# Kernel tuning notes

Measured on AMD Instinct MI355X. Metric: run time of the kernel, lower is better.

## Reference

```python
import jax, jax.numpy as jnp
import numpy as np

FP16_MIN = -65504.0
FP16_MAX = 65504.0

B, S, D, H = 2, 2048, 1024, 16
HD = D // H


def setup_inputs() -> dict:
    key = jax.random.key(0)
    ks = jax.random.split(key, 12)
    s = 0.02
    inp = {
        "x_q": jax.random.normal(ks[0], (B, S, D), jnp.float32),
        "x_k": jax.random.normal(ks[1], (B, S, D), jnp.float32),
        "x_v": jax.random.normal(ks[2], (B, S, D), jnp.float32),
        # causal mask [B, 1, S, S]; 0 entries are masked out
        "mask": jnp.broadcast_to(jnp.tril(jnp.ones((S, S), jnp.int32)), (B, 1, S, S)),
        "Wq": jax.random.normal(ks[3], (D, D), jnp.float32) * s,
        "bq": jnp.zeros((D,), jnp.float32),
        "Wk": jax.random.normal(ks[4], (D, D), jnp.float32) * s,
        "bk": jnp.zeros((D,), jnp.float32),
        "Wv": jax.random.normal(ks[5], (D, D), jnp.float32) * s,
        "bv": jnp.zeros((D,), jnp.float32),
        "Wo": jax.random.normal(ks[6], (D, D), jnp.float32) * s,
        "bo": jnp.zeros((D,), jnp.float32),
    }
    return inp


def _split_heads(x):
    # [B, S, D] -> [B, H, S, HD]
    b, s, _ = x.shape
    return x.reshape(b, s, H, HD).transpose(0, 2, 1, 3)


def reference(x_q, x_k, x_v, mask, Wq, bq, Wk, bk, Wv, bv, Wo, bo):
    scale = jnp.sqrt(jnp.float32(HD))
    q = _split_heads(x_q @ Wq + bq)  # [B,H,S,HD]
    k = _split_heads(x_k @ Wk + bk)
    v = _split_heads(x_v @ Wv + bv)

    scores = jnp.einsum("bhqd,bhkd->bhqk", q, k) / scale  # [B,H,S,S]
    scores = jnp.where(mask == 0, FP16_MIN, scores)
    scores = jnp.where(jnp.isneginf(scores), FP16_MIN, scores)
    scores = jnp.where(jnp.isposinf(scores), FP16_MAX, scores)

    probs = jax.nn.softmax(scores, axis=-1)  # dropout p=0.0 -> identity
    ctx = jnp.einsum("bhqk,bhkd->bhqd", probs, v)  # [B,H,S,HD]
    ctx = ctx.transpose(0, 2, 1, 3).reshape(x_q.shape[0], x_q.shape[1], D)
    out = ctx @ Wo + bo
    return out, probs
```

## Files before the change

kernel.cpp:

```cpp
#include <hip/hip_runtime.h>


typedef __bf16 bf16x8 __attribute__((ext_vector_type(8)));
typedef float f32x4 __attribute__((ext_vector_type(4)));

__device__ __forceinline__ unsigned short f2bf(float f) {
  unsigned int u = __builtin_bit_cast(unsigned int, f);
  u += 0x7fffu + ((u >> 16) & 1u);
  return (unsigned short)(u >> 16);
}
__device__ __forceinline__ unsigned short f2bf_hw(float f) {
  return __builtin_bit_cast(unsigned short, (__bf16)f);
}
__device__ __forceinline__ float bf2f_lo(unsigned int u) {
  return __builtin_bit_cast(float, u << 16);
}
__device__ __forceinline__ float bf2f_hi(unsigned int u) {
  return __builtin_bit_cast(float, u & 0xffff0000u);
}

__global__ void transpose_w(const float* __restrict__ W0, const float* __restrict__ W1,
                            const float* __restrict__ W2, const float* __restrict__ W3,
                            unsigned short* __restrict__ Wt) {
  __shared__ float t[32][33];
  const int z = blockIdx.z;
  const float* W = (z == 0) ? W0 : (z == 1) ? W1 : (z == 2) ? W2 : W3;
  unsigned short* o = Wt + (size_t)z * 1048576u;
  const int n0 = blockIdx.x * 32, k0 = blockIdx.y * 32;
  const int tx = threadIdx.x, ty = threadIdx.y;
#pragma unroll
  for (int i = 0; i < 4; i++)
    t[ty + 8 * i][tx] = W[(size_t)(k0 + ty + 8 * i) * 1024 + n0 + tx];
  __syncthreads();
#pragma unroll
  for (int i = 0; i < 4; i++)
    o[(size_t)(n0 + ty + 8 * i) * 1024 + k0 + tx] = f2bf(t[tx][ty + 8 * i]);
}

__global__ __launch_bounds__(256) void gemm_kernel(
    const void* __restrict__ A0, const void* __restrict__ A1, const void* __restrict__ A2,
    const unsigned short* __restrict__ Wtb,
    const float* __restrict__ b0, const float* __restrict__ b1, const float* __restrict__ b2,
    void* __restrict__ O0, void* __restrict__ O1, void* __restrict__ O2,
    const int mode0) {
  __shared__ unsigned short Alds[64 * 72];
  const int z = blockIdx.z;
  const int mode = mode0 + z;
  const void* Av = (z == 0) ? A0 : (z == 1) ? A1 : A2;
  const float* bias = (z == 0) ? b0 : (z == 1) ? b1 : b2;
  void* outv = (z == 0) ? O0 : (z == 1) ? O1 : O2;
  const unsigned short* Wt = Wtb + (size_t)z * 1048576u;

  const int tid = threadIdx.x;
  const int lane = tid & 63;
  const int wave = tid >> 6;
  const int wm = wave >> 1, wn = wave & 1;
  const int m0 = blockIdx.y * 64, n0 = blockIdx.x * 128;
  const int g = lane >> 4, c = lane & 15;

  f32x4 acc[2][4];
#pragma unroll
  for (int i = 0; i < 2; i++)
#pragma unroll
    for (int j = 0; j < 4; j++) acc[i][j] = (f32x4){0.f, 0.f, 0.f, 0.f};

  const int srow = tid >> 2;
  const int sch = (tid & 3) * 16;

  uint4 pk0, pk1;
#define LOAD_PACK(KB)                                                             \
  if (mode < 3) {                                                                 \
    const float* A = (const float*)Av;                                            \
    const float4* src = (const float4*)(A + (size_t)(m0 + srow) * 1024 + (KB) + sch); \
    const float4 v0 = src[0], v1 = src[1], v2 = src[2], v3 = src[3];              \
    pk0.x = (unsigned int)f2bf(v0.x) | ((unsigned int)f2bf(v0.y) << 16);          \
    pk0.y = (unsigned int)f2bf(v0.z) | ((unsigned int)f2bf(v0.w) << 16);          \
    pk0.z = (unsigned int)f2bf(v1.x) | ((unsigned int)f2bf(v1.y) << 16);          \
    pk0.w = (unsigned int)f2bf(v1.z) | ((unsigned int)f2bf(v1.w) << 16);          \
    pk1.x = (unsigned int)f2bf(v2.x) | ((unsigned int)f2bf(v2.y) << 16);          \
    pk1.y = (unsigned int)f2bf(v2.z) | ((unsigned int)f2bf(v2.w) << 16);          \
    pk1.z = (unsigned int)f2bf(v3.x) | ((unsigned int)f2bf(v3.y) << 16);          \
    pk1.w = (unsigned int)f2bf(v3.z) | ((unsigned int)f2bf(v3.w) << 16);          \
  } else {                                                                        \
    const unsigned short* A = (const unsigned short*)Av;                          \
    const uint4* src = (const uint4*)(A + (size_t)(m0 + srow) * 1024 + (KB) + sch); \
    pk0 = src[0];                                                                 \
    pk1 = src[1];                                                                 \
  }

  LOAD_PACK(0);
  for (int kb = 0; kb < 1024; kb += 64) {
    *(uint4*)&Alds[srow * 72 + sch] = pk0;
    *(uint4*)&Alds[srow * 72 + sch + 8] = pk1;
    if (kb + 64 < 1024) { LOAD_PACK(kb + 64); }
    __syncthreads();

    bf16x8 af[2][2], bfr[4][2];
#pragma unroll
    for (int mi = 0; mi < 2; mi++)
#pragma unroll
      for (int kk = 0; kk < 2; kk++)
        af[mi][kk] = *(const bf16x8*)&Alds[(wm * 32 + mi * 16 + c) * 72 + kk * 32 + g * 8];
#pragma unroll
    for (int nf = 0; nf < 4; nf++)
#pragma unroll
      for (int kk = 0; kk < 2; kk++)
        bfr[nf][kk] = *(const bf16x8*)(Wt + (size_t)(n0 + wn * 64 + nf * 16 + c) * 1024 + kb + kk * 32 + g * 8);
#pragma unroll
    for (int kk = 0; kk < 2; kk++)
#pragma unroll
      for (int mi = 0; mi < 2; mi++)
#pragma unroll
        for (int nf = 0; nf < 4; nf++)
          acc[mi][nf] = __builtin_amdgcn_mfma_f32_16x16x32_bf16(af[mi][kk], bfr[nf][kk], acc[mi][nf], 0, 0, 0);
    __syncthreads();
  }
#undef LOAD_PACK

#pragma unroll
  for (int nf = 0; nf < 4; nf++) {
    const int col = n0 + wn * 64 + nf * 16 + c;
    const float bc = bias[col];
#pragma unroll
    for (int mi = 0; mi < 2; mi++) {
#pragma unroll
      for (int r = 0; r < 4; r++) {
        const int row = m0 + wm * 32 + mi * 16 + g * 4 + r;
        const float v = acc[mi][nf][r] + bc;
        if (mode == 0) {
          ((unsigned short*)outv)[(size_t)row * 1024 + col] = f2bf(v * 0.1803368801111244f);
        } else if (mode == 1) {
          ((unsigned short*)outv)[(size_t)row * 1024 + col] = f2bf(v);
        } else if (mode == 2) {
          const int bb = row >> 11, s = row & 2047;
          ((unsigned short*)outv)[((size_t)(bb * 1024 + col)) * 2048 + s] = f2bf(v);
        } else {
          ((float*)outv)[(size_t)row * 1024 + col] = v;
        }
      }
    }
  }
}

__global__ __launch_bounds__(512, 4) void attn_kernel(
    const unsigned short* __restrict__ Q, const unsigned short* __restrict__ K,
    const unsigned short* __restrict__ Vt, float* __restrict__ probs,
    unsigned short* __restrict__ ctx) {
  __shared__ unsigned short Klds[2][64 * 72];
  __shared__ unsigned short Vlds[2][64 * 72];
  __shared__ unsigned short Plds[128 * 72];

  const int tid = threadIdx.x;
  const int lane = tid & 63, wave = tid >> 6;
  const int g = lane >> 4, c = lane & 15;
  const int bh = blockIdx.x;
  const int b = bh >> 4, h = bh & 15;
  const int q0 = (int)(gridDim.y - 1 - blockIdx.y) * 128;
  const int qrow0 = q0 + wave * 16;
  const int wave_kend = qrow0 + 16;

  const unsigned short* Qh = Q + ((size_t)(b * 2048 + qrow0)) * 1024 + h * 64;
  const unsigned short* Kh = K + ((size_t)b * 2048) * 1024 + h * 64;
  const unsigned short* Vh = Vt + ((size_t)bh) * 64 * 2048;
  float* Ph = probs + ((size_t)(bh * 2048 + q0)) * 2048;

  const bf16x8 qa0 = *(const bf16x8*)&Qh[(size_t)c * 1024 + g * 8];
  const bf16x8 qa1 = *(const bf16x8*)&Qh[(size_t)c * 1024 + 32 + g * 8];

  const int srow = tid >> 3;
  const int scol = (tid & 7) * 8;
  const int kb_end = q0 + 128;

  float lp[4] = {0.f, 0.f, 0.f, 0.f};
  f32x4 cacc[4];
#pragma unroll
  for (int nf = 0; nf < 4; nf++) cacc[nf] = (f32x4){0.f, 0.f, 0.f, 0.f};

  const int prow = lane >> 2;
  const int pcb = (lane & 3) * 16;
  unsigned short* PwOut = (unsigned short*)Ph + (size_t)(wave * 16 + prow) * 4096 + pcb;
  const unsigned short* PwLds = &Plds[(wave * 16 + prow) * 72 + pcb];

  {
    *(uint4*)&Klds[0][srow * 72 + scol] = *(const uint4*)(Kh + (size_t)srow * 1024 + scol);
    *(uint4*)&Vlds[0][srow * 72 + scol] = *(const uint4*)(Vh + (size_t)srow * 2048 + scol);
  }

  int cur = 0;
  for (int kb = 0; kb < kb_end; kb += 64, cur ^= 1) {
    uint4 kn, vn;
    const bool more = (kb + 64) < kb_end;
    if (more) {
      kn = *(const uint4*)(Kh + (size_t)(kb + 64 + srow) * 1024 + scol);
      vn = *(const uint4*)(Vh + (size_t)srow * 2048 + kb + 64 + scol);
    }
    __syncthreads();
    if (more) {
      *(uint4*)&Klds[cur ^ 1][srow * 72 + scol] = kn;
      *(uint4*)&Vlds[cur ^ 1][srow * 72 + scol] = vn;
    }

    if (kb < wave_kend) {
      f32x4 sv[4];
#pragma unroll
      for (int sub = 0; sub < 4; sub++) {
        sv[sub] = (f32x4){0.f, 0.f, 0.f, 0.f};
        const unsigned short* Kr = &Klds[cur][(sub * 16 + c) * 72];
        sv[sub] = __builtin_amdgcn_mfma_f32_16x16x32_bf16(qa0, *(const bf16x8*)&Kr[g * 8], sv[sub], 0, 0, 0);
        sv[sub] = __builtin_amdgcn_mfma_f32_16x16x32_bf16(qa1, *(const bf16x8*)&Kr[32 + g * 8], sv[sub], 0, 0, 0);
      }
      if (kb + 63 > qrow0) {
#pragma unroll
        for (int sub = 0; sub < 4; sub++)
#pragma unroll
          for (int r = 0; r < 4; r++)
            if (kb + sub * 16 + c > qrow0 + g * 4 + r) sv[sub][r] = -1e30f;
      }
#pragma unroll
      for (int sub = 0; sub < 4; sub++)
#pragma unroll
        for (int r = 0; r < 4; r++) {
          const float pu = __builtin_amdgcn_exp2f(sv[sub][r]);
          lp[r] += pu;
          Plds[(wave * 16 + g * 4 + r) * 72 + sub * 16 + c] = f2bf_hw(pu);
        }
      const bf16x8 pa0 = *(const bf16x8*)&Plds[(wave * 16 + c) * 72 + g * 8];
      const bf16x8 pa1 = *(const bf16x8*)&Plds[(wave * 16 + c) * 72 + 32 + g * 8];
#pragma unroll
      for (int nf = 0; nf < 4; nf++) {
        const bf16x8 vf0 = *(const bf16x8*)&Vlds[cur][(nf * 16 + c) * 72 + g * 8];
        const bf16x8 vf1 = *(const bf16x8*)&Vlds[cur][(nf * 16 + c) * 72 + 32 + g * 8];
        cacc[nf] = __builtin_amdgcn_mfma_f32_16x16x32_bf16(pa0, vf0, cacc[nf], 0, 0, 0);
        cacc[nf] = __builtin_amdgcn_mfma_f32_16x16x32_bf16(pa1, vf1, cacc[nf], 0, 0, 0);
      }
      unsigned short* dst = PwOut + kb;
      *(uint4*)dst = *(const uint4*)PwLds;
      *(uint4*)(dst + 8) = *(const uint4*)(PwLds + 8);
    } else {
      unsigned short* dst = PwOut + kb;
      *(uint4*)dst = make_uint4(0u, 0u, 0u, 0u);
      *(uint4*)(dst + 8) = make_uint4(0u, 0u, 0u, 0u);
    }
  }

#pragma unroll
  for (int off = 1; off < 16; off <<= 1)
#pragma unroll
    for (int r = 0; r < 4; r++) lp[r] += __shfl_xor(lp[r], off);
  float invl[4];
#pragma unroll
  for (int r = 0; r < 4; r++) invl[r] = 1.0f / lp[r];

#pragma unroll
  for (int nf = 0; nf < 4; nf++)
#pragma unroll
    for (int r = 0; r < 4; r++)
      ctx[((size_t)(b * 2048 + qrow0 + g * 4 + r)) * 1024 + h * 64 + nf * 16 + c] =
          f2bf_hw(cacc[nf][r] * invl[r]);
}

__global__ __launch_bounds__(256) void norm_probs(float* __restrict__ probs) {
  __shared__ float wsum[4];
  const int rowIdx = blockIdx.x;
  const int q = rowIdx & 2047;
  const int kbe = ((q >> 7) + 1) << 7;
  float* base = probs + (size_t)rowIdx * 2048;
  const int t = threadIdx.x;
  const int c0 = t * 8;

  uint4 raw = make_uint4(0u, 0u, 0u, 0u);
  if (c0 < kbe) raw = *(const uint4*)((const unsigned short*)base + c0);
  float f0 = bf2f_lo(raw.x), f1 = bf2f_hi(raw.x), f2 = bf2f_lo(raw.y), f3 = bf2f_hi(raw.y);
  float f4 = bf2f_lo(raw.z), f5 = bf2f_hi(raw.z), f6 = bf2f_lo(raw.w), f7 = bf2f_hi(raw.w);

  float s = ((f0 + f1) + (f2 + f3)) + ((f4 + f5) + (f6 + f7));
#pragma unroll
  for (int off = 1; off < 64; off <<= 1) s += __shfl_xor(s, off);
  if ((t & 63) == 0) wsum[t >> 6] = s;
  __syncthreads();
  const float il = 1.0f / (wsum[0] + wsum[1] + wsum[2] + wsum[3]);

  float4* dst = (float4*)(base + c0);
  dst[0] = make_float4(f0 * il, f1 * il, f2 * il, f3 * il);
  dst[1] = make_float4(f4 * il, f5 * il, f6 * il, f7 * il);
}

extern "C" void kernel_launch(void* const* d_in, const int* in_sizes, int n_in,
                              void* d_out, int out_size, void* d_ws, size_t ws_size,
                              hipStream_t stream) {
  if (ws_size < (size_t)40 * 1024 * 1024) return;

  const float* xq = (const float*)d_in[0];
  const float* xk = (const float*)d_in[1];
  const float* xv = (const float*)d_in[2];
  const float* Wq = (const float*)d_in[4];
  const float* bq = (const float*)d_in[5];
  const float* Wk = (const float*)d_in[6];
  const float* bk = (const float*)d_in[7];
  const float* Wv = (const float*)d_in[8];
  const float* bv = (const float*)d_in[9];
  const float* Wo = (const float*)d_in[10];
  const float* bo = (const float*)d_in[11];

  unsigned short* ws = (unsigned short*)d_ws;
  unsigned short* Wt = ws;
  unsigned short* Qw = ws + (size_t)4 * 1048576u;
  unsigned short* Kw = Qw + 4194304u;
  unsigned short* Vtw = Kw + 4194304u;
  unsigned short* Cw = Vtw + 4194304u;

  float* out = (float*)d_out;
  float* probs = out + 4194304u;

  transpose_w<<<dim3(32, 32, 4), dim3(32, 8), 0, stream>>>(Wq, Wk, Wv, Wo, Wt);
  gemm_kernel<<<dim3(8, 64, 3), 256, 0, stream>>>(xq, xk, xv, Wt, bq, bk, bv,
                                                  Qw, Kw, Vtw, 0);
  attn_kernel<<<dim3(32, 16, 1), 512, 0, stream>>>(Qw, Kw, Vtw, probs, Cw);
  norm_probs<<<dim3(65536), 256, 0, stream>>>(probs);
  gemm_kernel<<<dim3(8, 64, 1), 256, 0, stream>>>(Cw, Cw, Cw, Wt + 3u * 1048576u,
                                                  bo, bo, bo, out, out, out, 3);
}
```

Baseline: 353.6 us.

## Merge output projection GEMM with probs normalization into one launch

New measurement: 381.3 us. 7.8% more time.

```diff
diff --git a/kernel.cpp b/kernel.cpp
--- a/kernel.cpp
+++ b/kernel.cpp
@@ -37,18 +37,17 @@
     o[(size_t)(n0 + ty + 8 * i) * 1024 + k0 + tx] = f2bf(t[tx][ty + 8 * i]);
 }
 
-__global__ __launch_bounds__(256) void gemm_kernel(
-    const void* __restrict__ A0, const void* __restrict__ A1, const void* __restrict__ A2,
+__global__ __launch_bounds__(256) void gemm_qkv(
+    const float* __restrict__ A0, const float* __restrict__ A1, const float* __restrict__ A2,
     const unsigned short* __restrict__ Wtb,
     const float* __restrict__ b0, const float* __restrict__ b1, const float* __restrict__ b2,
-    void* __restrict__ O0, void* __restrict__ O1, void* __restrict__ O2,
-    const int mode0) {
+    unsigned short* __restrict__ O0, unsigned short* __restrict__ O1,
+    unsigned short* __restrict__ O2) {
   __shared__ unsigned short Alds[64 * 72];
   const int z = blockIdx.z;
-  const int mode = mode0 + z;
-  const void* Av = (z == 0) ? A0 : (z == 1) ? A1 : A2;
+  const float* A = (z == 0) ? A0 : (z == 1) ? A1 : A2;
   const float* bias = (z == 0) ? b0 : (z == 1) ? b1 : b2;
-  void* outv = (z == 0) ? O0 : (z == 1) ? O1 : O2;
+  unsigned short* outv = (z == 0) ? O0 : (z == 1) ? O1 : O2;
   const unsigned short* Wt = Wtb + (size_t)z * 1048576u;
 
   const int tid = threadIdx.x;
@@ -69,8 +68,7 @@
 
   uint4 pk0, pk1;
 #define LOAD_PACK(KB)                                                             \
-  if (mode < 3) {                                                                 \
-    const float* A = (const float*)Av;                                            \
+  {                                                                               \
     const float4* src = (const float4*)(A + (size_t)(m0 + srow) * 1024 + (KB) + sch); \
     const float4 v0 = src[0], v1 = src[1], v2 = src[2], v3 = src[3];              \
     pk0.x = (unsigned int)f2bf(v0.x) | ((unsigned int)f2bf(v0.y) << 16);          \
@@ -81,11 +79,6 @@
     pk1.y = (unsigned int)f2bf(v2.z) | ((unsigned int)f2bf(v2.w) << 16);          \
     pk1.z = (unsigned int)f2bf(v3.x) | ((unsigned int)f2bf(v3.y) << 16);          \
     pk1.w = (unsigned int)f2bf(v3.z) | ((unsigned int)f2bf(v3.w) << 16);          \
-  } else {                                                                        \
-    const unsigned short* A = (const unsigned short*)Av;                          \
-    const uint4* src = (const uint4*)(A + (size_t)(m0 + srow) * 1024 + (KB) + sch); \
-    pk0 = src[0];                                                                 \
-    pk1 = src[1];                                                                 \
   }
 
   LOAD_PACK(0);
@@ -127,15 +120,13 @@
       for (int r = 0; r < 4; r++) {
         const int row = m0 + wm * 32 + mi * 16 + g * 4 + r;
         const float v = acc[mi][nf][r] + bc;
-        if (mode == 0) {
-          ((unsigned short*)outv)[(size_t)row * 1024 + col] = f2bf(v * 0.1803368801111244f);
-        } else if (mode == 1) {
-          ((unsigned short*)outv)[(size_t)row * 1024 + col] = f2bf(v);
-        } else if (mode == 2) {
+        if (z == 0) {
+          outv[(size_t)row * 1024 + col] = f2bf(v * 0.1803368801111244f);
+        } else if (z == 1) {
+          outv[(size_t)row * 1024 + col] = f2bf(v);
+        } else {
           const int bb = row >> 11, s = row & 2047;
-          ((unsigned short*)outv)[((size_t)(bb * 1024 + col)) * 2048 + s] = f2bf(v);
-        } else {
-          ((float*)outv)[(size_t)row * 1024 + col] = v;
+          outv[((size_t)(bb * 1024 + col)) * 2048 + s] = f2bf(v);
         }
       }
     }
@@ -259,30 +250,97 @@
           f2bf_hw(cacc[nf][r] * invl[r]);
 }
 
-__global__ __launch_bounds__(256) void norm_probs(float* __restrict__ probs) {
-  __shared__ float wsum[4];
-  const int rowIdx = blockIdx.x;
-  const int q = rowIdx & 2047;
-  const int kbe = ((q >> 7) + 1) << 7;
-  float* base = probs + (size_t)rowIdx * 2048;
-  const int t = threadIdx.x;
-  const int c0 = t * 8;
-
-  uint4 raw = make_uint4(0u, 0u, 0u, 0u);
-  if (c0 < kbe) raw = *(const uint4*)((const unsigned short*)base + c0);
-  float f0 = bf2f_lo(raw.x), f1 = bf2f_hi(raw.x), f2 = bf2f_lo(raw.y), f3 = bf2f_hi(raw.y);
-  float f4 = bf2f_lo(raw.z), f5 = bf2f_hi(raw.z), f6 = bf2f_lo(raw.w), f7 = bf2f_hi(raw.w);
-
-  float s = ((f0 + f1) + (f2 + f3)) + ((f4 + f5) + (f6 + f7));
-#pragma unroll
-  for (int off = 1; off < 64; off <<= 1) s += __shfl_xor(s, off);
-  if ((t & 63) == 0) wsum[t >> 6] = s;
-  __syncthreads();
-  const float il = 1.0f / (wsum[0] + wsum[1] + wsum[2] + wsum[3]);
-
-  float4* dst = (float4*)(base + c0);
-  dst[0] = make_float4(f0 * il, f1 * il, f2 * il, f3 * il);
-  dst[1] = make_float4(f4 * il, f5 * il, f6 * il, f7 * il);
+__global__ __launch_bounds__(256) void norm_out(
+    float* __restrict__ probs,
+    const unsigned short* __restrict__ Cw, const unsigned short* __restrict__ Wt,
+    const float* __restrict__ bo, float* __restrict__ out) {
+  __shared__ unsigned short sh[64 * 72];
+  const int tid = threadIdx.x;
+
+  if (blockIdx.x < 512) {
+    const int lane = tid & 63;
+    const int wave = tid >> 6;
+    const int wm = wave >> 1, wn = wave & 1;
+    const int m0 = (int)(blockIdx.x >> 3) * 64, n0 = (int)(blockIdx.x & 7) * 128;
+    const int g = lane >> 4, c = lane & 15;
+
+    f32x4 acc[2][4];
+#pragma unroll
+    for (int i = 0; i < 2; i++)
+#pragma unroll
+      for (int j = 0; j < 4; j++) acc[i][j] = (f32x4){0.f, 0.f, 0.f, 0.f};
+
+    const int srow = tid >> 2;
+    const int sch = (tid & 3) * 16;
+
+    uint4 pk0 = *(const uint4*)(Cw + (size_t)(m0 + srow) * 1024 + sch);
+    uint4 pk1 = *(const uint4*)(Cw + (size_t)(m0 + srow) * 1024 + sch + 8);
+    for (int kb = 0; kb < 1024; kb += 64) {
+      *(uint4*)&sh[srow * 72 + sch] = pk0;
+      *(uint4*)&sh[srow * 72 + sch + 8] = pk1;
+      if (kb + 64 < 1024) {
+        pk0 = *(const uint4*)(Cw + (size_t)(m0 + srow) * 1024 + kb + 64 + sch);
+        pk1 = *(const uint4*)(Cw + (size_t)(m0 + srow) * 1024 + kb + 64 + sch + 8);
+      }
+      __syncthreads();
+
+      bf16x8 af[2][2], bfr[4][2];
+#pragma unroll
+      for (int mi = 0; mi < 2; mi++)
+#pragma unroll
+        for (int kk = 0; kk < 2; kk++)
+          af[mi][kk] = *(const bf16x8*)&sh[(wm * 32 + mi * 16 + c) * 72 + kk * 32 + g * 8];
+#pragma unroll
+      for (int nf = 0; nf < 4; nf++)
+#pragma unroll
+        for (int kk = 0; kk < 2; kk++)
+          bfr[nf][kk] = *(const bf16x8*)(Wt + (size_t)(n0 + wn * 64 + nf * 16 + c) * 1024 + kb + kk * 32 + g * 8);
+#pragma unroll
+      for (int kk = 0; kk < 2; kk++)
+#pragma unroll
+        for (int mi = 0; mi < 2; mi++)
+#pragma unroll
+          for (int nf = 0; nf < 4; nf++)
+            acc[mi][nf] = __builtin_amdgcn_mfma_f32_16x16x32_bf16(af[mi][kk], bfr[nf][kk], acc[mi][nf], 0, 0, 0);
+      __syncthreads();
+    }
+
+#pragma unroll
+    for (int nf = 0; nf < 4; nf++) {
+      const int col = n0 + wn * 64 + nf * 16 + c;
+      const float bc = bo[col];
+#pragma unroll
+      for (int mi = 0; mi < 2; mi++)
+#pragma unroll
+        for (int r = 0; r < 4; r++) {
+          const int row = m0 + wm * 32 + mi * 16 + g * 4 + r;
+          out[(size_t)row * 1024 + col] = acc[mi][nf][r] + bc;
+        }
+    }
+  } else {
+    float* wsum = (float*)sh;
+    const int rowIdx = (int)blockIdx.x - 512;
+    const int q = rowIdx & 2047;
+    const int kbe = ((q >> 7) + 1) << 7;
+    float* base = probs + (size_t)rowIdx * 2048;
+    const int c0 = tid * 8;
+
+    uint4 raw = make_uint4(0u, 0u, 0u, 0u);
+    if (c0 < kbe) raw = *(const uint4*)((const unsigned short*)base + c0);
+    float f0 = bf2f_lo(raw.x), f1 = bf2f_hi(raw.x), f2 = bf2f_lo(raw.y), f3 = bf2f_hi(raw.y);
+    float f4 = bf2f_lo(raw.z), f5 = bf2f_hi(raw.z), f6 = bf2f_lo(raw.w), f7 = bf2f_hi(raw.w);
+
+    float s = ((f0 + f1) + (f2 + f3)) + ((f4 + f5) + (f6 + f7));
+#pragma unroll
+    for (int off = 1; off < 64; off <<= 1) s += __shfl_xor(s, off);
+    if ((tid & 63) == 0) wsum[tid >> 6] = s;
+    __syncthreads();
+    const float il = 1.0f / (wsum[0] + wsum[1] + wsum[2] + wsum[3]);
+
+    float4* dst = (float4*)(base + c0);
+    dst[0] = make_float4(f0 * il, f1 * il, f2 * il, f3 * il);
+    dst[1] = make_float4(f4 * il, f5 * il, f6 * il, f7 * il);
+  }
 }
 
 extern "C" void kernel_launch(void* const* d_in, const int* in_sizes, int n_in,
@@ -313,10 +371,9 @@
   float* probs = out + 4194304u;
 
   transpose_w<<<dim3(32, 32, 4), dim3(32, 8), 0, stream>>>(Wq, Wk, Wv, Wo, Wt);
-  gemm_kernel<<<dim3(8, 64, 3), 256, 0, stream>>>(xq, xk, xv, Wt, bq, bk, bv,
-                                                  Qw, Kw, Vtw, 0);
+  gemm_qkv<<<dim3(8, 64, 3), 256, 0, stream>>>(xq, xk, xv, Wt, bq, bk, bv,
+                                               Qw, Kw, Vtw);
   attn_kernel<<<dim3(32, 16, 1), 512, 0, stream>>>(Qw, Kw, Vtw, probs, Cw);
-  norm_probs<<<dim3(65536), 256, 0, stream>>>(probs);
-  gemm_kernel<<<dim3(8, 64, 1), 256, 0, stream>>>(Cw, Cw, Cw, Wt + 3u * 1048576u,
-                                                  bo, bo, bo, out, out, out, 3);
-}
+  norm_out<<<dim3(512 + 65536), 256, 0, stream>>>(probs, Cw, Wt + 3u * 1048576u,
+                                                  bo, out);
+}
```
